# Performance work log

Measured on AMD Instinct MI355X. Metric: run time of the kernel, lower is better.

The kernel has to match this reference:

```python
import jax, jax.numpy as jnp
import numpy as np

B, T, ROLL, RHY, COND, Z1, H = 4096, 32, 130, 3, 12, 128, 1024
IN1 = Z1 + ROLL + RHY + COND  # 273, grucell_1 input size


def _gru_cell(x, h, w_ih, w_hh, b_ih, b_hh):
    # PyTorch GRUCell math. w_ih: [3H, in], w_hh: [3H, H]
    gi = x @ w_ih.T + b_ih
    gh = h @ w_hh.T + b_hh
    i_r, i_z, i_n = jnp.split(gi, 3, axis=1)
    h_r, h_z, h_n = jnp.split(gh, 3, axis=1)
    r = jax.nn.sigmoid(i_r + h_r)
    z = jax.nn.sigmoid(i_z + h_z)
    n = jnp.tanh(i_n + r * h_n)
    return (1.0 - z) * n + z * h


def setup_inputs() -> dict:
    key = jax.random.key(0)
    ks = jax.random.split(key, 20)
    s = 0.02
    inp = {
        "z1": jax.random.normal(ks[0], (B, Z1), jnp.float32),
        "dis1_mean": jax.random.normal(ks[1], (B, Z1), jnp.float32),
        "dis1_std": jax.random.uniform(ks[2], (B, Z1), jnp.float32),
        "dis2_mean": jax.random.normal(ks[3], (B, Z1), jnp.float32),
        "dis2_std": jax.random.uniform(ks[4], (B, Z1), jnp.float32),
        "recon_rhythm": jax.random.normal(ks[5], (B, T, RHY), jnp.float32),
        "sample": jax.random.normal(ks[6], (B, T, ROLL), jnp.float32),
        "condition": jax.random.normal(ks[7], (B, T, COND), jnp.float32),
        "iteration": 1000,
        # grucell_1
        "w_ih1": jax.random.normal(ks[8], (3 * H, IN1), jnp.float32) * s,
        "w_hh1": jax.random.normal(ks[9], (3 * H, H), jnp.float32) * s,
        "b_ih1": jax.random.normal(ks[10], (3 * H,), jnp.float32) * s,
        "b_hh1": jax.random.normal(ks[11], (3 * H,), jnp.float32) * s,
        # grucell_2
        "w_ih2": jax.random.normal(ks[12], (3 * H, H), jnp.float32) * s,
        "w_hh2": jax.random.normal(ks[13], (3 * H, H), jnp.float32) * s,
        "b_ih2": jax.random.normal(ks[14], (3 * H,), jnp.float32) * s,
        "b_hh2": jax.random.normal(ks[15], (3 * H,), jnp.float32) * s,
        # linear_init_1: z1 -> H
        "w_init": jax.random.normal(ks[16], (H, Z1), jnp.float32) * s,
        "b_init": jax.random.normal(ks[17], (H,), jnp.float32) * s,
        # linear_out_1: H -> roll
        "w_out": jax.random.normal(ks[18], (ROLL, H), jnp.float32) * s,
        "b_out": jax.random.normal(ks[19], (ROLL,), jnp.float32) * s,
    }
    return inp


def reference(z1, dis1_mean, dis1_std, dis2_mean, dis2_std, recon_rhythm, sample,
              condition, iteration, w_ih1, w_hh1, b_ih1, b_hh1, w_ih2, w_hh2,
              b_ih2, b_hh2, w_init, b_init, w_out, b_out):
    # Eval-mode final_decoder: teacher forcing off, argmax one-hot sampling.
    h1_0 = jnp.tanh(z1 @ w_init.T + b_init)
    out0 = jnp.zeros((B, ROLL), z1.dtype).at[:, -1].set(1.0)
    h2_0 = jnp.zeros((B, H), z1.dtype)  # overwritten at step 0

    rhy_t = jnp.transpose(recon_rhythm, (1, 0, 2))   # [T,B,RHY]
    cond_t = jnp.transpose(condition, (1, 0, 2))     # [T,B,COND]

    def step(carry, xs):
        out, h1, h2 = carry
        i, r_i, c_i = xs
        inp = jnp.concatenate([out, r_i, z1, c_i], axis=1)  # [B, IN1]
        h1 = _gru_cell(inp, h1, w_ih1, w_hh1, b_ih1, b_hh1)
        h2 = jnp.where(i == 0, h1, h2)  # hx[1] = hx[0] on first step
        h2 = _gru_cell(h1, h2, w_ih2, w_hh2, b_ih2, b_hh2)
        logp = jax.nn.log_softmax(h2 @ w_out.T + b_out, axis=1)  # [B,ROLL]
        out = jax.nn.one_hot(jnp.argmax(logp, axis=1), ROLL, dtype=logp.dtype)
        return (out, h1, h2), logp

    xs = (jnp.arange(T), rhy_t, cond_t)
    _, logps = jax.lax.scan(step, (out0, h1_0, h2_0), xs)
    recon = jnp.transpose(logps, (1, 0, 2))  # [B,T,ROLL]
    return (recon, recon_rhythm, dis1_mean, dis1_std, dis2_mean, dis2_std)
```

## Files before the change

### kernel.cpp

```cpp
#include <hip/hip_runtime.h>
#include <stdint.h>

typedef unsigned short u16;
typedef unsigned int u32;
typedef __attribute__((ext_vector_type(4))) float f32x4;
typedef __attribute__((ext_vector_type(8))) short short8;

#define MFMA16(a, b, c) __builtin_amdgcn_mfma_f32_16x16x32_bf16(a, b, c, 0, 0, 0)

#define B_SZ   4096
#define H_SZ   1024
#define T_SZ   32
#define NROLL  130
#define EXTK   192
#define NCPAD  144

__device__ __forceinline__ u16 f2b(float f) {
  u32 u = __float_as_uint(f);
  u += 0x7FFFu + ((u >> 16) & 1u);
  return (u16)(u >> 16);
}
__device__ __forceinline__ float sigm(float x) { return 1.f / (1.f + __expf(-x)); }

__device__ __forceinline__ void gld16(const void* g, const void* lds) {
  __builtin_amdgcn_global_load_lds(
      (const __attribute__((address_space(1))) u32*)(uintptr_t)g,
      (__attribute__((address_space(3))) u32*)(u32)(uintptr_t)lds, 16, 0, 0);
}

__global__ void cvt_kernel(const float* __restrict__ s, u16* __restrict__ d, int n) {
  int i = blockIdx.x * 256 + threadIdx.x;
  if (i < n) d[i] = f2b(s[i]);
}

__global__ void build_wout_kernel(const float* __restrict__ w, u16* __restrict__ d) {
  int i = blockIdx.x * 256 + threadIdx.x;
  int r = i >> 10, c = i & 1023;
  d[i] = f2b(r < NROLL ? w[r * H_SZ + c] : 0.f);
}

__global__ void build_wext_kernel(const float* __restrict__ w, u16* __restrict__ d) {
  int i = blockIdx.x * 256 + threadIdx.x;
  int j = i / EXTK, k = i % EXTK;
  float v = 0.f;
  if (k < 3)        v = w[j * 273 + 130 + k];
  else if (k < 15)  v = w[j * 273 + 261 + (k - 3)];
  else if (k < 143) v = w[j * 273 + 133 + (k - 15)];
  d[i] = f2b(v);
}

__global__ void build_wih1T_kernel(const float* __restrict__ w, float* __restrict__ d) {
  int i = blockIdx.x * 256 + threadIdx.x;
  if (i >= NROLL * 3072) return;
  int c = i / 3072, j = i % 3072;
  d[i] = w[j * 273 + c];
}

__global__ void build_aext_kernel(const float* __restrict__ rhy, const float* __restrict__ cond,
                                  const float* __restrict__ z1, u16* __restrict__ d) {
  long long i = (long long)blockIdx.x * 256 + threadIdx.x;
  int t = (int)(i / (B_SZ * EXTK));
  int r = (int)(i % (B_SZ * EXTK));
  int b = r / EXTK, k = r % EXTK;
  float v = 0.f;
  if (k < 3)        v = rhy[b * (T_SZ * 3) + t * 3 + k];
  else if (k < 15)  v = cond[b * (T_SZ * 12) + t * 12 + (k - 3)];
  else if (k < 143) v = z1[b * 128 + (k - 15)];
  d[i] = f2b(v);
}

__global__ void init_amax_kernel(int* __restrict__ a) {
  a[blockIdx.x * 256 + threadIdx.x] = NROLL - 1;
}

__global__ __launch_bounds__(256, 2)
void init_h1_mfma_kernel(const u16* __restrict__ Az,
                         const u16* __restrict__ Wz,
                         const float* __restrict__ b_init,
                         float* __restrict__ h1f, u16* __restrict__ h1b) {
  __shared__ u16 As[128 * 64];
  __shared__ u16 Ws[64 * 64];
  const int tid = threadIdx.x;
  const int lane = tid & 63, wv = tid >> 6;
  const int wm = wv >> 1, wn = wv & 1;
  const int lr = lane & 15, lk = lane >> 4;
  const int Mbase = blockIdx.x * 128, Nbase = blockIdx.y * 64;

  f32x4 zero = {0.f, 0.f, 0.f, 0.f};
  f32x4 acc[4][2];
#pragma unroll
  for (int m = 0; m < 4; ++m)
#pragma unroll
    for (int n = 0; n < 2; ++n) acc[m][n] = zero;

  for (int it = 0; it < 2; ++it) {
#pragma unroll
    for (int i = 0; i < 4; ++i) {
      int seg = i * 256 + tid, row = seg >> 3, c8 = seg & 7;
      gld16(Az + (size_t)(Mbase + row) * 128 + it * 64 + c8 * 8, As + ((i * 256 + (wv << 6)) << 3));
    }
#pragma unroll
    for (int i = 0; i < 2; ++i) {
      int seg = i * 256 + tid, row = seg >> 3, c8 = seg & 7;
      gld16(Wz + (size_t)(Nbase + row) * 128 + it * 64 + c8 * 8, Ws + ((i * 256 + (wv << 6)) << 3));
    }
    __syncthreads();
#pragma unroll
    for (int kk = 0; kk < 2; ++kk) {
      short8 af[4];
#pragma unroll
      for (int m = 0; m < 4; ++m)
        af[m] = *(const short8*)(As + (((wm << 6) + (m << 4) + lr) << 6) + kk * 32 + (lk << 3));
      short8 bw[2];
#pragma unroll
      for (int n = 0; n < 2; ++n)
        bw[n] = *(const short8*)(Ws + ((((wn << 5) + (n << 4) + lr)) << 6) + kk * 32 + (lk << 3));
#pragma unroll
      for (int m = 0; m < 4; ++m)
#pragma unroll
        for (int n = 0; n < 2; ++n)
          acc[m][n] = MFMA16(af[m], bw[n], acc[m][n]);
    }
    __syncthreads();
  }

  int hcol[2];
  hcol[0] = Nbase + (wn << 5) + lr;
  hcol[1] = hcol[0] + 16;
#pragma unroll
  for (int m = 0; m < 4; ++m) {
#pragma unroll
    for (int q = 0; q < 4; ++q) {
      int b = Mbase + (wm << 6) + (m << 4) + (lk << 2) + q;
      size_t ho = (size_t)b << 10;
#pragma unroll
      for (int n = 0; n < 2; ++n) {
        int h = hcol[n];
        float v = tanhf(acc[m][n][q] + b_init[h]);
        h1f[ho + h] = v;
        h1b[ho + h] = f2b(v);
      }
    }
  }
}

__global__ __launch_bounds__(256, 2)
void gru1_kernel(const u16* __restrict__ Ah,
                 const u16* __restrict__ Whh,
                 const u16* __restrict__ Ae,
                 const u16* __restrict__ Wex,
                 const float* __restrict__ gT,
                 const float* __restrict__ bih, const float* __restrict__ bhh,
                 const int* __restrict__ amax,
                 float* __restrict__ h1f, u16* __restrict__ h1o) {
  __shared__ u16 smem[40960];
  u16* As = smem;
  u16* Wsm = smem + 16384;
  const int tid = threadIdx.x;
  const int lane = tid & 63, wv = tid >> 6;
  const int wm = wv >> 1, wn = wv & 1;
  const int lr = lane & 15, lk = lane >> 4;
  const int Mbase = blockIdx.x * 128, Nbase = blockIdx.y * 64;

  f32x4 zero = {0.f, 0.f, 0.f, 0.f};
  f32x4 acc_r[4][2], acc_z[4][2], acc_hn[4][2], acc_in[4][2];
#pragma unroll
  for (int m = 0; m < 4; ++m)
#pragma unroll
    for (int n = 0; n < 2; ++n) { acc_r[m][n] = zero; acc_z[m][n] = zero; acc_hn[m][n] = zero; acc_in[m][n] = zero; }

#pragma unroll 1
  for (int it = 0; it < 8; ++it) {
#pragma unroll
    for (int i = 0; i < 8; ++i) {
      int seg = i * 256 + tid, row = seg >> 4, c16 = (seg & 15) ^ (row & 7);
      gld16(Ah + (size_t)(Mbase + row) * 1024 + it * 128 + c16 * 8, As + ((i * 256 + (wv << 6)) << 3));
    }
#pragma unroll
    for (int i = 0; i < 12; ++i) {
      int seg = i * 256 + tid, gr = seg >> 4, c16 = (seg & 15) ^ (gr & 7);
      int gg = gr >> 6, r = gr & 63;
      gld16(Whh + ((size_t)(gg << 10) + Nbase + r) * 1024 + it * 128 + c16 * 8,
            Wsm + ((i * 256 + (wv << 6)) << 3));
    }
    __syncthreads();
#pragma unroll
    for (int kk = 0; kk < 4; ++kk) {
      int gc = (kk << 2) + lk;
      short8 af[4];
#pragma unroll
      for (int m = 0; m < 4; ++m) {
        int row = (wm << 6) + (m << 4) + lr;
        af[m] = *(const short8*)(As + (row << 7) + ((gc ^ (row & 7)) << 3));
      }
      short8 bw[3][2];
#pragma unroll
      for (int g = 0; g < 3; ++g)
#pragma unroll
        for (int n = 0; n < 2; ++n) {
          int row = (g << 6) + (wn << 5) + (n << 4) + lr;
          bw[g][n] = *(const short8*)(Wsm + (row << 7) + ((gc ^ (row & 7)) << 3));
        }
#pragma unroll
      for (int m = 0; m < 4; ++m)
#pragma unroll
        for (int n = 0; n < 2; ++n) {
          acc_r[m][n] = MFMA16(af[m], bw[0][n], acc_r[m][n]);
          acc_z[m][n] = MFMA16(af[m], bw[1][n], acc_z[m][n]);
          acc_hn[m][n] = MFMA16(af[m], bw[2][n], acc_hn[m][n]);
        }
    }
    __syncthreads();
  }

#pragma unroll 1
  for (int e = 0; e < 3; ++e) {
#pragma unroll
    for (int i = 0; i < 4; ++i) {
      int seg = i * 256 + tid, row = seg >> 3, c8 = (seg & 7) ^ (row & 7);
      gld16(Ae + (size_t)(Mbase + row) * EXTK + e * 64 + c8 * 8, As + ((i * 256 + (wv << 6)) << 3));
    }
#pragma unroll
    for (int i = 0; i < 6; ++i) {
      int seg = i * 256 + tid, gr = seg >> 3, c8 = (seg & 7) ^ (gr & 7);
      int gg = gr >> 6, r = gr & 63;
      gld16(Wex + ((size_t)(gg << 10) + Nbase + r) * EXTK + e * 64 + c8 * 8,
            Wsm + ((i * 256 + (wv << 6)) << 3));
    }
    __syncthreads();
#pragma unroll
    for (int kk = 0; kk < 2; ++kk) {
      int gc = (kk << 2) + lk;
      short8 af[4];
#pragma unroll
      for (int m = 0; m < 4; ++m) {
        int row = (wm << 6) + (m << 4) + lr;
        af[m] = *(const short8*)(As + (row << 6) + ((gc ^ (row & 7)) << 3));
      }
      short8 bw[3][2];
#pragma unroll
      for (int g = 0; g < 3; ++g)
#pragma unroll
        for (int n = 0; n < 2; ++n) {
          int row = (g << 6) + (wn << 5) + (n << 4) + lr;
          bw[g][n] = *(const short8*)(Wsm + (row << 6) + ((gc ^ (row & 7)) << 3));
        }
#pragma unroll
      for (int m = 0; m < 4; ++m)
#pragma unroll
        for (int n = 0; n < 2; ++n) {
          acc_r[m][n] = MFMA16(af[m], bw[0][n], acc_r[m][n]);
          acc_z[m][n] = MFMA16(af[m], bw[1][n], acc_z[m][n]);
          acc_in[m][n] = MFMA16(af[m], bw[2][n], acc_in[m][n]);
        }
    }
    __syncthreads();
  }

  int hcol[2];
  hcol[0] = Nbase + (wn << 5) + lr;
  hcol[1] = hcol[0] + 16;
  float bi0[2], bi1[2], bi2[2], bh0[2], bh1[2], bh2[2];
#pragma unroll
  for (int n = 0; n < 2; ++n) {
    int h = hcol[n];
    bi0[n] = bih[h]; bi1[n] = bih[1024 + h]; bi2[n] = bih[2048 + h];
    bh0[n] = bhh[h]; bh1[n] = bhh[1024 + h]; bh2[n] = bhh[2048 + h];
  }
#pragma unroll
  for (int m = 0; m < 4; ++m) {
#pragma unroll
    for (int q = 0; q < 4; ++q) {
      int b = Mbase + (wm << 6) + (m << 4) + (lk << 2) + q;
      const float* gRow = gT + (size_t)amax[b] * 3072;
      size_t ho = (size_t)b << 10;
#pragma unroll
      for (int n = 0; n < 2; ++n) {
        int h = hcol[n];
        float rp = acc_r[m][n][q] + bi0[n] + bh0[n] + gRow[h];
        float zp = acc_z[m][n][q] + bi1[n] + bh1[n] + gRow[1024 + h];
        float inp = acc_in[m][n][q] + bi2[n] + gRow[2048 + h];
        float hnp = acc_hn[m][n][q] + bh2[n];
        float r = sigm(rp), z = sigm(zp);
        float nn = tanhf(inp + r * hnp);
        float hv = (1.f - z) * nn + z * h1f[ho + h];
        h1f[ho + h] = hv;
        h1o[ho + h] = f2b(hv);
      }
    }
  }
}

__global__ __launch_bounds__(256, 2)
void gru2_kernel(const u16* __restrict__ A1,
                 const u16* __restrict__ A2,
                 const u16* __restrict__ Wi,
                 const u16* __restrict__ Wh,
                 const float* __restrict__ bih, const float* __restrict__ bhh,
                 const float* __restrict__ hpf,
                 float* __restrict__ h2f, u16* __restrict__ h2o) {
  __shared__ u16 As1[128 * 64];
  __shared__ u16 As2[128 * 64];
  __shared__ u16 Ws[384 * 64];
  const int tid = threadIdx.x;
  const int lane = tid & 63, wv = tid >> 6;
  const int wm = wv >> 1, wn = wv & 1;
  const int lr = lane & 15, lk = lane >> 4;
  const int Mbase = blockIdx.x * 128, Nbase = blockIdx.y * 64;

  f32x4 zero = {0.f, 0.f, 0.f, 0.f};
  f32x4 acc_r[4][2], acc_z[4][2], acc_hn[4][2], acc_in[4][2];
#pragma unroll
  for (int m = 0; m < 4; ++m)
#pragma unroll
    for (int n = 0; n < 2; ++n) { acc_r[m][n] = zero; acc_z[m][n] = zero; acc_hn[m][n] = zero; acc_in[m][n] = zero; }

#pragma unroll 1
  for (int it = 0; it < 16; ++it) {
#pragma unroll
    for (int i = 0; i < 4; ++i) {
      int seg = i * 256 + tid, row = seg >> 3, c8 = (seg & 7) ^ (row & 7);
      size_t go = (size_t)(Mbase + row) * 1024 + it * 64 + c8 * 8;
      gld16(A1 + go, As1 + ((i * 256 + (wv << 6)) << 3));
      gld16(A2 + go, As2 + ((i * 256 + (wv << 6)) << 3));
    }
#pragma unroll
    for (int i = 0; i < 12; ++i) {
      int seg = i * 256 + tid, gr = seg >> 3, c8 = (seg & 7) ^ (gr & 7);
      int s = gr >> 6, r = gr & 63;
      const u16* Wm = (s < 3) ? Wi : Wh;
      int gate = (s < 3) ? s : (s - 3);
      gld16(Wm + ((size_t)(gate << 10) + Nbase + r) * 1024 + it * 64 + c8 * 8,
            Ws + ((i * 256 + (wv << 6)) << 3));
    }
    __syncthreads();
#pragma unroll
    for (int kk = 0; kk < 2; ++kk) {
      int gc = (kk << 2) + lk;
      short8 a1[4], a2[4];
#pragma unroll
      for (int m = 0; m < 4; ++m) {
        int row = (wm << 6) + (m << 4) + lr;
        int off = (row << 6) + ((gc ^ (row & 7)) << 3);
        a1[m] = *(const short8*)(As1 + off);
        a2[m] = *(const short8*)(As2 + off);
      }
      short8 bw[6][2];
#pragma unroll
      for (int s = 0; s < 6; ++s)
#pragma unroll
        for (int n = 0; n < 2; ++n) {
          int row = (s << 6) + (wn << 5) + (n << 4) + lr;
          bw[s][n] = *(const short8*)(Ws + (row << 6) + ((gc ^ (row & 7)) << 3));
        }
#pragma unroll
      for (int m = 0; m < 4; ++m)
#pragma unroll
        for (int n = 0; n < 2; ++n) {
          acc_r[m][n] = MFMA16(a1[m], bw[0][n], acc_r[m][n]);
          acc_r[m][n] = MFMA16(a2[m], bw[3][n], acc_r[m][n]);
          acc_z[m][n] = MFMA16(a1[m], bw[1][n], acc_z[m][n]);
          acc_z[m][n] = MFMA16(a2[m], bw[4][n], acc_z[m][n]);
          acc_in[m][n] = MFMA16(a1[m], bw[2][n], acc_in[m][n]);
          acc_hn[m][n] = MFMA16(a2[m], bw[5][n], acc_hn[m][n]);
        }
    }
    __syncthreads();
  }

  int hcol[2];
  hcol[0] = Nbase + (wn << 5) + lr;
  hcol[1] = hcol[0] + 16;
  float bi0[2], bi1[2], bi2[2], bh0[2], bh1[2], bh2[2];
#pragma unroll
  for (int n = 0; n < 2; ++n) {
    int h = hcol[n];
    bi0[n] = bih[h]; bi1[n] = bih[1024 + h]; bi2[n] = bih[2048 + h];
    bh0[n] = bhh[h]; bh1[n] = bhh[1024 + h]; bh2[n] = bhh[2048 + h];
  }
#pragma unroll
  for (int m = 0; m < 4; ++m) {
#pragma unroll
    for (int q = 0; q < 4; ++q) {
      int b = Mbase + (wm << 6) + (m << 4) + (lk << 2) + q;
      size_t ho = (size_t)b << 10;
#pragma unroll
      for (int n = 0; n < 2; ++n) {
        int h = hcol[n];
        float r = sigm(acc_r[m][n][q] + bi0[n] + bh0[n]);
        float z = sigm(acc_z[m][n][q] + bi1[n] + bh1[n]);
        float nn = tanhf(acc_in[m][n][q] + bi2[n] + r * (acc_hn[m][n][q] + bh2[n]));
        float hv = (1.f - z) * nn + z * hpf[ho + h];
        h2f[ho + h] = hv;
        h2o[ho + h] = f2b(hv);
      }
    }
  }
}

__global__ __launch_bounds__(256)
void out_kernel(const u16* __restrict__ A,
                const u16* __restrict__ W,
                const float* __restrict__ b_out,
                float* __restrict__ recon, int* __restrict__ amax_out, int t) {
  __shared__ u16 As[64 * 64];
  __shared__ u16 Ws[160 * 64];
  const int tid = threadIdx.x;
  const int lane = tid & 63, wv = tid >> 6;
  const int lr = lane & 15, lk = lane >> 4;
  const int bb = blockIdx.x;

  f32x4 zero = {0.f, 0.f, 0.f, 0.f};
  f32x4 acc[9];
#pragma unroll
  for (int n = 0; n < 9; ++n) acc[n] = zero;

#pragma unroll 1
  for (int it = 0; it < 16; ++it) {
#pragma unroll
    for (int i = 0; i < 2; ++i) {
      int seg = i * 256 + tid, row = seg >> 3, c8 = seg & 7;
      gld16(A + (size_t)(bb * 64 + row) * 1024 + it * 64 + c8 * 8, As + ((i * 256 + (wv << 6)) << 3));
    }
#pragma unroll
    for (int i = 0; i < 4; ++i) {
      int seg = i * 256 + tid, row = seg >> 3, c8 = seg & 7;
      gld16(W + (size_t)row * 1024 + it * 64 + c8 * 8, Ws + ((i * 256 + (wv << 6)) << 3));
    }
    if (wv < 2) {
      int seg = 4 * 256 + tid, row = seg >> 3, c8 = seg & 7;
      gld16(W + (size_t)row * 1024 + it * 64 + c8 * 8, Ws + ((4 * 256 + (wv << 6)) << 3));
    }
    __syncthreads();
#pragma unroll
    for (int kk = 0; kk < 2; ++kk) {
      short8 af = *(const short8*)(As + (((wv << 4) + lr) << 6) + kk * 32 + (lk << 3));
#pragma unroll
      for (int n = 0; n < 9; ++n) {
        short8 bw = *(const short8*)(Ws + ((((n << 4) + lr)) << 6) + kk * 32 + (lk << 3));
        acc[n] = MFMA16(af, bw, acc[n]);
      }
    }
    __syncthreads();
  }

#pragma unroll
  for (int q = 0; q < 4; ++q) {
    int b = bb * 64 + (wv << 4) + (lk << 2) + q;
    float v[9];
    float vmax = -1e30f; int vidx = 0;
#pragma unroll
    for (int n = 0; n < 9; ++n) {
      int col = (n << 4) + lr;
      float x = acc[n][q];
      x = (col < NROLL) ? (x + b_out[col]) : -1e30f;
      v[n] = x;
      if (x > vmax) { vmax = x; vidx = col; }
    }
    for (int d = 1; d < 16; d <<= 1) {
      float om = __shfl_xor(vmax, d);
      int oi = __shfl_xor(vidx, d);
      if (om > vmax || (om == vmax && oi < vidx)) { vmax = om; vidx = oi; }
    }
    float s = 0.f;
#pragma unroll
    for (int n = 0; n < 9; ++n) s += __expf(v[n] - vmax);
    for (int d = 1; d < 16; d <<= 1) s += __shfl_xor(s, d);
    float logZ = vmax + __logf(s);
#pragma unroll
    for (int n = 0; n < 9; ++n) {
      int col = (n << 4) + lr;
      if (col < NROLL) recon[(size_t)b * (T_SZ * NROLL) + t * NROLL + col] = v[n] - logZ;
    }
    if (lr == 0) amax_out[b] = vidx;
  }
}

extern "C" void kernel_launch(void* const* d_in, const int* in_sizes, int n_in,
                              void* d_out, int out_size, void* d_ws, size_t ws_size,
                              hipStream_t stream) {
  const float* z1    = (const float*)d_in[0];
  const float* d1m   = (const float*)d_in[1];
  const float* d1s   = (const float*)d_in[2];
  const float* d2m   = (const float*)d_in[3];
  const float* d2s   = (const float*)d_in[4];
  const float* rhy   = (const float*)d_in[5];
  const float* cond  = (const float*)d_in[7];
  const float* w_ih1 = (const float*)d_in[9];
  const float* w_hh1 = (const float*)d_in[10];
  const float* b_ih1 = (const float*)d_in[11];
  const float* b_hh1 = (const float*)d_in[12];
  const float* w_ih2 = (const float*)d_in[13];
  const float* w_hh2 = (const float*)d_in[14];
  const float* b_ih2 = (const float*)d_in[15];
  const float* b_hh2 = (const float*)d_in[16];
  const float* w_init = (const float*)d_in[17];
  const float* b_init = (const float*)d_in[18];
  const float* w_out  = (const float*)d_in[19];
  const float* b_out  = (const float*)d_in[20];
  float* out = (float*)d_out;

  char* ws = (char*)d_ws;
  size_t off = 0;
  auto alloc = [&](size_t bytes) -> void* {
    off = (off + 255) & ~(size_t)255;
    void* p = ws + off;
    off += bytes;
    return p;
  };
  u16* whh1_b = (u16*)alloc((size_t)3072 * 1024 * 2);
  u16* wih2_b = (u16*)alloc((size_t)3072 * 1024 * 2);
  u16* whh2_b = (u16*)alloc((size_t)3072 * 1024 * 2);
  u16* wout_b = (u16*)alloc((size_t)NCPAD * 1024 * 2);
  u16* wext_b = (u16*)alloc((size_t)3072 * EXTK * 2);
  float* wih1T = (float*)alloc((size_t)NROLL * 3072 * 4);
  u16* aext   = (u16*)alloc((size_t)T_SZ * B_SZ * EXTK * 2);
  float* h1f  = (float*)alloc((size_t)B_SZ * H_SZ * 4);
  float* h2f  = (float*)alloc((size_t)B_SZ * H_SZ * 4);
  u16* h1b[2];
  h1b[0] = (u16*)alloc((size_t)B_SZ * H_SZ * 2);
  h1b[1] = (u16*)alloc((size_t)B_SZ * H_SZ * 2);
  u16* h2b[2];
  h2b[0] = (u16*)alloc((size_t)B_SZ * H_SZ * 2);
  h2b[1] = (u16*)alloc((size_t)B_SZ * H_SZ * 2);
  int* amax = (int*)alloc((size_t)B_SZ * 4);
  u16* z1b    = (u16*)alloc((size_t)B_SZ * 128 * 2);
  u16* winitb = (u16*)alloc((size_t)H_SZ * 128 * 2);

  const int NW = 3072 * 1024;
  cvt_kernel<<<(NW + 255) / 256, 256, 0, stream>>>(w_hh1, whh1_b, NW);
  cvt_kernel<<<(NW + 255) / 256, 256, 0, stream>>>(w_ih2, wih2_b, NW);
  cvt_kernel<<<(NW + 255) / 256, 256, 0, stream>>>(w_hh2, whh2_b, NW);
  cvt_kernel<<<(B_SZ * 128 + 255) / 256, 256, 0, stream>>>(z1, z1b, B_SZ * 128);
  cvt_kernel<<<(H_SZ * 128 + 255) / 256, 256, 0, stream>>>(w_init, winitb, H_SZ * 128);
  build_wout_kernel<<<(NCPAD * 1024) / 256, 256, 0, stream>>>(w_out, wout_b);
  build_wext_kernel<<<(3072 * EXTK) / 256, 256, 0, stream>>>(w_ih1, wext_b);
  build_wih1T_kernel<<<(NROLL * 3072 + 255) / 256, 256, 0, stream>>>(w_ih1, wih1T);
  build_aext_kernel<<<(T_SZ * B_SZ * EXTK) / 256, 256, 0, stream>>>(rhy, cond, z1, aext);
  init_h1_mfma_kernel<<<dim3(B_SZ / 128, H_SZ / 64), 256, 0, stream>>>(z1b, winitb, b_init, h1f, h1b[0]);
  init_amax_kernel<<<B_SZ / 256, 256, 0, stream>>>(amax);

  size_t o_rhy = (size_t)B_SZ * T_SZ * NROLL;
  size_t o_d1m = o_rhy + (size_t)B_SZ * T_SZ * 3;
  size_t o_d1s = o_d1m + (size_t)B_SZ * 128;
  size_t o_d2m = o_d1s + (size_t)B_SZ * 128;
  size_t o_d2s = o_d2m + (size_t)B_SZ * 128;
  hipMemcpyAsync(out + o_rhy, rhy, (size_t)B_SZ * T_SZ * 3 * 4, hipMemcpyDeviceToDevice, stream);
  hipMemcpyAsync(out + o_d1m, d1m, (size_t)B_SZ * 128 * 4, hipMemcpyDeviceToDevice, stream);
  hipMemcpyAsync(out + o_d1s, d1s, (size_t)B_SZ * 128 * 4, hipMemcpyDeviceToDevice, stream);
  hipMemcpyAsync(out + o_d2m, d2m, (size_t)B_SZ * 128 * 4, hipMemcpyDeviceToDevice, stream);
  hipMemcpyAsync(out + o_d2s, d2s, (size_t)B_SZ * 128 * 4, hipMemcpyDeviceToDevice, stream);

  dim3 ggrid(B_SZ / 128, H_SZ / 64);
  for (int t = 0; t < T_SZ; ++t) {
    const u16* h1in = h1b[t & 1];
    u16* h1out = h1b[(t & 1) ^ 1];
    gru1_kernel<<<ggrid, 256, 0, stream>>>(h1in, whh1_b, aext + (size_t)t * B_SZ * EXTK,
                                           wext_b, wih1T, b_ih1, b_hh1, amax, h1f, h1out);
    const u16* h2in = (t == 0) ? (const u16*)h1out : h2b[t & 1];
    const float* hpf = (t == 0) ? h1f : h2f;
    u16* h2out = h2b[(t & 1) ^ 1];
    gru2_kernel<<<ggrid, 256, 0, stream>>>(h1out, h2in, wih2_b, whh2_b, b_ih2, b_hh2,
                                           hpf, h2f, h2out);
    out_kernel<<<B_SZ / 64, 256, 0, stream>>>(h2out, wout_b, b_out, out, amax, t);
  }
  (void)in_sizes; (void)n_in; (void)out_size; (void)ws_size;
}
```

Baseline: 3.891 ms.

## Raise wave priority around MFMA loops and split out_kernel columns across waves

Wraps the MFMA compute sections of both GRU kernels in s_setprio(1)/s_setprio(0) so waves doing matrix math are favoured over waves issuing loads. Restructures out_kernel to use 16 batch rows per block with 2 waves splitting the 9 column fragments (5/4). A shared-memory cross-wave reduction then combines max, argmax and log-sum-exp. This launches 4x more blocks to raise parallelism in the small output GEMM, at the cost of reloading the output weight tile in 4x more blocks and an extra block barrier.

```diff
diff --git a/kernel.cpp b/kernel.cpp
--- a/kernel.cpp
+++ b/kernel.cpp
@@ -184,6 +184,7 @@
             Wsm + ((i * 256 + (wv << 6)) << 3));
     }
     __syncthreads();
+    __builtin_amdgcn_s_setprio(1);
 #pragma unroll
     for (int kk = 0; kk < 4; ++kk) {
       int gc = (kk << 2) + lk;
@@ -210,6 +211,7 @@
           acc_hn[m][n] = MFMA16(af[m], bw[2][n], acc_hn[m][n]);
         }
     }
+    __builtin_amdgcn_s_setprio(0);
     __syncthreads();
   }
 
@@ -228,6 +230,7 @@
             Wsm + ((i * 256 + (wv << 6)) << 3));
     }
     __syncthreads();
+    __builtin_amdgcn_s_setprio(1);
 #pragma unroll
     for (int kk = 0; kk < 2; ++kk) {
       int gc = (kk << 2) + lk;
@@ -254,6 +257,7 @@
           acc_in[m][n] = MFMA16(af[m], bw[2][n], acc_in[m][n]);
         }
     }
+    __builtin_amdgcn_s_setprio(0);
     __syncthreads();
   }
 
@@ -334,6 +338,7 @@
             Ws + ((i * 256 + (wv << 6)) << 3));
     }
     __syncthreads();
+    __builtin_amdgcn_s_setprio(1);
 #pragma unroll
     for (int kk = 0; kk < 2; ++kk) {
       int gc = (kk << 2) + lk;
@@ -365,6 +370,7 @@
           acc_hn[m][n] = MFMA16(a2[m], bw[5][n], acc_hn[m][n]);
         }
     }
+    __builtin_amdgcn_s_setprio(0);
     __syncthreads();
   }
 
@@ -398,47 +404,55 @@
   }
 }
 
-__global__ __launch_bounds__(256)
+__global__ __launch_bounds__(128)
 void out_kernel(const u16* __restrict__ A,
                 const u16* __restrict__ W,
                 const float* __restrict__ b_out,
                 float* __restrict__ recon, int* __restrict__ amax_out, int t) {
-  __shared__ u16 As[64 * 64];
-  __shared__ u16 Ws[160 * 64];
+  __shared__ u16 As[16 * 64];
+  __shared__ u16 Ws[144 * 64];
+  __shared__ float redm[2][16], reds[2][16], logZs[16];
+  __shared__ int redi[2][16];
   const int tid = threadIdx.x;
   const int lane = tid & 63, wv = tid >> 6;
   const int lr = lane & 15, lk = lane >> 4;
   const int bb = blockIdx.x;
+  const int nf0 = wv ? 5 : 0;
+  const int nfn = wv ? 4 : 5;
 
   f32x4 zero = {0.f, 0.f, 0.f, 0.f};
-  f32x4 acc[9];
-#pragma unroll
-  for (int n = 0; n < 9; ++n) acc[n] = zero;
+  f32x4 acc[5];
+#pragma unroll
+  for (int j = 0; j < 5; ++j) acc[j] = zero;
+
+  float bo[5];
+#pragma unroll
+  for (int j = 0; j < 5; ++j) {
+    int col = ((nf0 + j) << 4) + lr;
+    bo[j] = (j < nfn && col < NROLL) ? b_out[col] : -1e30f;
+  }
 
 #pragma unroll 1
   for (int it = 0; it < 16; ++it) {
-#pragma unroll
-    for (int i = 0; i < 2; ++i) {
-      int seg = i * 256 + tid, row = seg >> 3, c8 = seg & 7;
-      gld16(A + (size_t)(bb * 64 + row) * 1024 + it * 64 + c8 * 8, As + ((i * 256 + (wv << 6)) << 3));
-    }
-#pragma unroll
-    for (int i = 0; i < 4; ++i) {
-      int seg = i * 256 + tid, row = seg >> 3, c8 = seg & 7;
-      gld16(W + (size_t)row * 1024 + it * 64 + c8 * 8, Ws + ((i * 256 + (wv << 6)) << 3));
-    }
-    if (wv < 2) {
-      int seg = 4 * 256 + tid, row = seg >> 3, c8 = seg & 7;
-      gld16(W + (size_t)row * 1024 + it * 64 + c8 * 8, Ws + ((4 * 256 + (wv << 6)) << 3));
+    {
+      int seg = tid, row = seg >> 3, c8 = seg & 7;
+      gld16(A + (size_t)(bb * 16 + row) * 1024 + it * 64 + c8 * 8, As + ((wv << 6) << 3));
+    }
+#pragma unroll
+    for (int i = 0; i < 9; ++i) {
+      int seg = i * 128 + tid, row = seg >> 3, c8 = seg & 7;
+      gld16(W + (size_t)row * 1024 + it * 64 + c8 * 8, Ws + ((i * 128 + (wv << 6)) << 3));
     }
     __syncthreads();
 #pragma unroll
     for (int kk = 0; kk < 2; ++kk) {
-      short8 af = *(const short8*)(As + (((wv << 4) + lr) << 6) + kk * 32 + (lk << 3));
-#pragma unroll
-      for (int n = 0; n < 9; ++n) {
-        short8 bw = *(const short8*)(Ws + ((((n << 4) + lr)) << 6) + kk * 32 + (lk << 3));
-        acc[n] = MFMA16(af, bw, acc[n]);
+      short8 af = *(const short8*)(As + (lr << 6) + kk * 32 + (lk << 3));
+#pragma unroll 5
+      for (int j = 0; j < 5; ++j) {
+        if (j < nfn) {
+          short8 bw = *(const short8*)(Ws + ((((nf0 + j) << 4) + lr) << 6) + kk * 32 + (lk << 3));
+          acc[j] = MFMA16(af, bw, acc[j]);
+        }
       }
     }
     __syncthreads();
@@ -446,16 +460,15 @@
 
 #pragma unroll
   for (int q = 0; q < 4; ++q) {
-    int b = bb * 64 + (wv << 4) + (lk << 2) + q;
-    float v[9];
+    int r = (lk << 2) + q;
     float vmax = -1e30f; int vidx = 0;
-#pragma unroll
-    for (int n = 0; n < 9; ++n) {
-      int col = (n << 4) + lr;
-      float x = acc[n][q];
-      x = (col < NROLL) ? (x + b_out[col]) : -1e30f;
-      v[n] = x;
-      if (x > vmax) { vmax = x; vidx = col; }
+#pragma unroll 5
+    for (int j = 0; j < 5; ++j) {
+      if (j < nfn) {
+        int col = ((nf0 + j) << 4) + lr;
+        float x = acc[j][q] + bo[j];
+        if (x > vmax) { vmax = x; vidx = col; }
+      }
     }
     for (int d = 1; d < 16; d <<= 1) {
       float om = __shfl_xor(vmax, d);
@@ -463,16 +476,38 @@
       if (om > vmax || (om == vmax && oi < vidx)) { vmax = om; vidx = oi; }
     }
     float s = 0.f;
-#pragma unroll
-    for (int n = 0; n < 9; ++n) s += __expf(v[n] - vmax);
+#pragma unroll 5
+    for (int j = 0; j < 5; ++j) {
+      if (j < nfn) s += __expf(acc[j][q] + bo[j] - vmax);
+    }
     for (int d = 1; d < 16; d <<= 1) s += __shfl_xor(s, d);
-    float logZ = vmax + __logf(s);
-#pragma unroll
-    for (int n = 0; n < 9; ++n) {
-      int col = (n << 4) + lr;
-      if (col < NROLL) recon[(size_t)b * (T_SZ * NROLL) + t * NROLL + col] = v[n] - logZ;
-    }
-    if (lr == 0) amax_out[b] = vidx;
+    if (lr == 0) { redm[wv][r] = vmax; reds[wv][r] = s; redi[wv][r] = vidx; }
+  }
+  __syncthreads();
+
+  if (tid < 16) {
+    float m0 = redm[0][tid], m1 = redm[1][tid];
+    float s0 = reds[0][tid], s1 = reds[1][tid];
+    float M = fmaxf(m0, m1);
+    float S = s0 * __expf(m0 - M) + s1 * __expf(m1 - M);
+    logZs[tid] = M + __logf(S);
+    amax_out[bb * 16 + tid] = (m1 > m0) ? redi[1][tid] : redi[0][tid];
+  }
+  __syncthreads();
+
+#pragma unroll
+  for (int q = 0; q < 4; ++q) {
+    int r = (lk << 2) + q;
+    int b = bb * 16 + r;
+    float lz = logZs[r];
+#pragma unroll 5
+    for (int j = 0; j < 5; ++j) {
+      if (j < nfn) {
+        int col = ((nf0 + j) << 4) + lr;
+        if (col < NROLL)
+          recon[(size_t)b * (T_SZ * NROLL) + t * NROLL + col] = acc[j][q] + bo[j] - lz;
+      }
+    }
   }
 }
 
@@ -562,7 +597,7 @@
     u16* h2out = h2b[(t & 1) ^ 1];
     gru2_kernel<<<ggrid, 256, 0, stream>>>(h1out, h2in, wih2_b, whh2_b, b_ih2, b_hh2,
                                            hpf, h2f, h2out);
-    out_kernel<<<B_SZ / 64, 256, 0, stream>>>(h2out, wout_b, b_out, out, amax, t);
+    out_kernel<<<B_SZ / 16, 128, 0, stream>>>(h2out, wout_b, b_out, out, amax, t);
   }
   (void)in_sizes; (void)n_in; (void)out_size; (void)ws_size;
 }
```

Measured after the change: 3.663 ms. 1.06x faster.
